# Optimization experiments

Hardware: AMD Instinct MI355X
Metric: run time of the kernel (lower is better)

The kernel has to match this reference:

```python
import jax, jax.numpy as jnp
import numpy as np

N, C, H, W, K = 8, 32, 512, 512, 6   # batch, embed dim, image HW, max components per image
MIN_PIX = 20
EPS = 1e-6
MARGIN = 0.5
L_INTER, L_INST, L_BG, L_SCENE = 0.4, 0.1, 0.2, 0.5


def _build_labels():
    # K disjoint 'subtitle line' rectangles per image; label 0 = background.
    # This is exactly what cv2.connectedComponents would return on the gt mask.
    labels = np.zeros((N, H, W), np.int32)
    for n in range(N):
        for k in range(K):
            r0 = 30 + k * 75
            c0 = 60 + (n % 3) * 20
            labels[n, r0:r0 + 40, c0:c0 + 300] = k + 1
    return labels


def setup_inputs() -> dict:
    key = jax.random.key(0)
    k1, k2 = jax.random.split(key)
    labels = _build_labels()
    gt = (labels > 0).astype(np.float32)[:, None]          # [N,1,H,W]
    color = jax.random.normal(k1, (N, C, H, W), jnp.float32)
    binary = jax.random.uniform(k2, (N, 1, H, W), jnp.float32)  # pred binary map
    return {"color": color, "gt": jnp.asarray(gt), "binary": binary,
            "comp_labels": jnp.asarray(labels)}


def _safe_norm(d2):
    # torch.norm = sqrt(sum sq); tiny floor avoids NaN grads at exactly 0
    return jnp.sqrt(jnp.maximum(d2, 1e-12))


def reference(color, gt, binary, comp_labels):
    f32 = color.dtype
    sub = (gt[:, 0] > 0.5).astype(f32)                                   # [N,H,W]
    text = (jax.lax.stop_gradient(binary)[:, 0] > 0.5).astype(f32)       # detached
    scene = text * (1.0 - sub)
    bg = (1.0 - sub) * (1.0 - scene)

    # one-hot component masks [N,K,H,W]
    comp = (comp_labels[:, None, :, :] ==
            jnp.arange(1, K + 1, dtype=comp_labels.dtype)[None, :, None, None]).astype(f32)
    cnt = comp.sum((2, 3))                                               # [N,K]

    # per-component first/second moments via batched segment-reduce
    S1 = jnp.einsum('nchw,nkhw->nkc', color, comp)                       # sum of feat
    fsq = (color * color).sum(1)                                         # [N,H,W]
    S2 = jnp.einsum('nhw,nkhw->nk', fsq, comp)                           # sum of |feat|^2
    m_inst = S1 / (cnt + EPS)[:, :, None]                                # [N,K,C]
    # sum over comp pixels of |f - m|^2, divided by (cnt+eps)
    intra_k = (S2 - 2.0 * (m_inst * S1).sum(-1)
               + cnt * (m_inst * m_inst).sum(-1)) / (cnt + EPS)

    sub_cnt = sub.sum((1, 2)); bg_cnt = bg.sum((1, 2)); scene_cnt = scene.sum((1, 2))
    m_sub = jnp.einsum('nchw,nhw->nc', color, sub) / (sub_cnt + EPS)[:, None]
    m_bg = jnp.einsum('nchw,nhw->nc', color, bg) / (bg_cnt + EPS)[:, None]
    m_scene = jnp.einsum('nchw,nhw->nc', color, scene) / (scene_cnt + EPS)[:, None]

    comp_big = cnt >= MIN_PIX                                            # [N,K]
    n_valid = comp_big.sum(1)                                            # [N]
    item_valid = (bg_cnt >= MIN_PIX) & (n_valid >= 1)
    cv = comp_big & item_valid[:, None]
    total = cv.sum()

    intra_sum = jnp.where(cv, intra_k, 0.0).sum()

    d_inst_bg = _safe_norm(((m_inst - m_bg[:, None, :]) ** 2).sum(-1))   # [N,K]
    inter_sum = jnp.where(cv, jax.nn.relu(MARGIN - d_inst_bg) ** 2, 0.0).sum()

    item_multi = item_valid & (n_valid > 1)
    d2_inst_sub = ((m_inst - m_sub[:, None, :]) ** 2).sum(-1)
    inst_sum = jnp.where(cv & item_multi[:, None], d2_inst_sub, 0.0).sum()
    inst_n = jnp.where(item_multi, n_valid, 0).sum()

    bg_cond = item_valid & (sub_cnt >= MIN_PIX)
    d_sub_bg = _safe_norm(((m_sub - m_bg) ** 2).sum(-1))
    subbg_sum = jnp.where(bg_cond, jax.nn.relu(MARGIN - d_sub_bg) ** 2, 0.0).sum()
    subbg_n = bg_cond.sum()

    sc_cond = item_valid & (scene_cnt >= MIN_PIX) & (sub_cnt >= MIN_PIX)
    d_sub_sc = _safe_norm(((m_sub - m_scene) ** 2).sum(-1))
    subsc_sum = jnp.where(sc_cond, jax.nn.relu(2.0 * MARGIN - d_sub_sc) ** 2, 0.0).sum()
    subsc_n = sc_cond.sum()

    def avg(s, n):
        return jnp.where(n > 0, s / jnp.maximum(n, 1).astype(f32), 0.0)

    loss = (avg(intra_sum, total)
            + L_INTER * avg(inter_sum, total)
            + L_INST * avg(inst_sum, inst_n)
            + L_BG * avg(subbg_sum, subbg_n)
            + L_SCENE * avg(subsc_sum, subsc_n))
    return jnp.where(total > 0, loss, jnp.zeros((), f32))
```

## Files before the change

### kernel.cpp

```cpp
#include <hip/hip_runtime.h>


#define NIMG   8
#define NCH    32
#define IMHW   (512 * 512)
#define CHUNK  1024
#define CPI    (IMHW / CHUNK)
#define WSN    304
#define LC_OFF    12288
#define CODES_OFF 16384

__device__ __forceinline__ float redhalf(float x) {
    x += __shfl_xor(x, 1);  x += __shfl_xor(x, 2);  x += __shfl_xor(x, 4);
    x += __shfl_xor(x, 8);  x += __shfl_xor(x, 16);
    return x;
}
__device__ __forceinline__ float red64(float x) {
    x = redhalf(x); x += __shfl_xor(x, 32); return x;
}

__global__ __launch_bounds__(256) void scl_codes(
    const float* __restrict__ gt, const float* __restrict__ bin,
    const int* __restrict__ lab, float* __restrict__ ws,
    unsigned char* __restrict__ lc, unsigned* __restrict__ codes)
{
    __shared__ float ldsc[8];
    __shared__ int labmask;
    const int tid = threadIdx.x;
    if (tid < 8) ldsc[tid] = 0.f;
    if (tid == 0) labmask = 0;

    const int n = blockIdx.x / CPI;
    const int q = blockIdx.x % CPI;
    const int base = n * IMHW + q * CHUNK;
    const int p = base + (tid << 2);

    const float4 g4 = *reinterpret_cast<const float4*>(gt + p);
    const float4 b4 = *reinterpret_cast<const float4*>(bin + p);
    const int4   l4 = *reinterpret_cast<const int4*>(lab + p);
    const float gg[4] = {g4.x, g4.y, g4.z, g4.w};
    const float bb[4] = {b4.x, b4.y, b4.z, b4.w};
    const int   ll[4] = {l4.x, l4.y, l4.z, l4.w};

    unsigned wrd = 0; int lm = 0;
    float c0 = 0.f, c1 = 0.f;
    float ck[6] = {0.f, 0.f, 0.f, 0.f, 0.f, 0.f};
#pragma unroll
    for (int e = 0; e < 4; ++e) {
        const bool sub  = gg[e] > 0.5f;
        const bool text = bb[e] > 0.5f;
        const int  r    = sub ? 0 : (text ? 1 : 2);
        unsigned   ul   = (unsigned)ll[e];
        if (ul > 7u) ul = 7u;
        wrd |= ((ul << 2) | (unsigned)r) << (8 * e);
        lm  |= 1 << ul;
        c0  += (r == 0) ? 1.f : 0.f;
        c1  += (r == 1) ? 1.f : 0.f;
#pragma unroll
        for (int kk = 0; kk < 6; ++kk)
            ck[kk] += (ul == (unsigned)(kk + 1)) ? 1.f : 0.f;
    }
    codes[(base >> 2) + tid] = wrd;

    c0 = red64(c0); c1 = red64(c1);
#pragma unroll
    for (int kk = 0; kk < 6; ++kk) ck[kk] = red64(ck[kk]);
    lm |= __shfl_xor(lm, 1);  lm |= __shfl_xor(lm, 2);  lm |= __shfl_xor(lm, 4);
    lm |= __shfl_xor(lm, 8);  lm |= __shfl_xor(lm, 16); lm |= __shfl_xor(lm, 32);

    __syncthreads();
    if ((tid & 63) == 0) {
        atomicAdd(&ldsc[0], c0);
        atomicAdd(&ldsc[1], c1);
#pragma unroll
        for (int kk = 0; kk < 6; ++kk) atomicAdd(&ldsc[2 + kk], ck[kk]);
        atomicOr(&labmask, lm);
    }
    __syncthreads();

    float* wsn = ws + (size_t)n * WSN;
    if (tid == 0) {
        lc[n * CPI + q] = (unsigned char)((labmask >> 1) & 0x3F);
        atomicAdd(&wsn[288], ldsc[0]);
        atomicAdd(&wsn[289], ldsc[1]);
    }
    if (tid >= 2 && tid < 8) atomicAdd(&wsn[291 + (tid - 2)], ldsc[tid]);
}

__global__ __launch_bounds__(256) void scl_color(
    const float* __restrict__ color, const float* __restrict__ ws_ro,
    const unsigned char* __restrict__ lc, const unsigned* __restrict__ codes,
    float* __restrict__ ws)
{
    __shared__ unsigned ldsC[CHUNK / 4];
    (void)ws_ro;

    const int bid = blockIdx.x;
    const int g = bid & 3;
    const int q = (bid >> 2) & (CPI - 1);
    const int n = bid >> 10;

    const int tid  = threadIdx.x;
    const int lane = tid & 63;
    const int wv   = tid >> 6;
    const int half = lane >> 5;
    const int l32  = lane & 31;

    const int base = n * IMHW + q * CHUNK;
    ldsC[tid] = codes[(base >> 2) + tid];

    const unsigned mask6 = lc[n * CPI + q];
    const int Lc = mask6 ? __ffs(mask6) : 255;

    const int c = g * 8 + wv * 2 + half;
    const float* colc = color + ((size_t)n * NCH + c) * IMHW + q * CHUNK;

    __syncthreads();

    float vt = 0.f, s0 = 0.f, s1 = 0.f, aL = 0.f, s2 = 0.f;
#pragma unroll
    for (int j = 0; j < CHUNK; j += 128) {
        const int off = j + (l32 << 2);
        const float4 v4 = *reinterpret_cast<const float4*>(colc + off);
        const unsigned cw = ldsC[off >> 2];
        const float vv[4] = {v4.x, v4.y, v4.z, v4.w};
#pragma unroll
        for (int e = 0; e < 4; ++e) {
            const float v = vv[e];
            const int r = (int)((cw >> (8 * e)) & 3u);
            const int l = (int)((cw >> (8 * e + 2)) & 0x3Fu);
            vt += v;
            s0 += (r == 0) ? v : 0.f;
            s1 += (r == 1) ? v : 0.f;
            const float mv = (l == Lc) ? v : 0.f;
            aL += mv;
            s2 = fmaf(mv, mv, s2);
        }
    }

    vt = redhalf(vt); s0 = redhalf(s0); s1 = redhalf(s1);
    aL = redhalf(aL); s2 = redhalf(s2);
    s2 += __shfl_xor(s2, 32);

    float* wsn = ws + (size_t)n * WSN;
    if (l32 == 0) {
        atomicAdd(&wsn[ 0 + c], s0);
        atomicAdd(&wsn[32 + c], s1);
        atomicAdd(&wsn[64 + c], vt);
        if (Lc >= 1 && Lc <= 6) {
            atomicAdd(&wsn[96 + (Lc - 1) * 32 + c], aL);
            if (lane == 0) atomicAdd(&wsn[297 + (Lc - 1)], s2);
        }
    }

    unsigned extra = mask6 ? (mask6 & (mask6 - 1)) : 0u;
    while (extra) {
        const int L2 = __ffs(extra); extra &= extra - 1;
        float aX = 0.f, sX = 0.f;
#pragma unroll
        for (int j = 0; j < CHUNK; j += 128) {
            const int off = j + (l32 << 2);
            const float4 v4 = *reinterpret_cast<const float4*>(colc + off);
            const unsigned cw = ldsC[off >> 2];
            const float vv[4] = {v4.x, v4.y, v4.z, v4.w};
#pragma unroll
            for (int e = 0; e < 4; ++e) {
                const int l = (int)((cw >> (8 * e + 2)) & 0x3Fu);
                const float mv = (l == L2) ? vv[e] : 0.f;
                aX += mv;
                sX = fmaf(mv, mv, sX);
            }
        }
        aX = redhalf(aX); sX = redhalf(sX);
        sX += __shfl_xor(sX, 32);
        if (l32 == 0 && L2 >= 1 && L2 <= 6) {
            atomicAdd(&wsn[96 + (L2 - 1) * 32 + c], aX);
            if (lane == 0) atomicAdd(&wsn[297 + (L2 - 1)], sX);
        }
    }
}

__global__ void scl_final(const float* __restrict__ ws, float* __restrict__ out)
{
    const int lane = threadIdx.x;
    const int n = lane / 6;
    const int k = lane - n * 6;
    const bool active = lane < 48;

    float t_cv = 0.f, t_intra = 0.f, t_inter = 0.f, t_inst = 0.f, t_instn = 0.f;
    float t_sbg = 0.f, t_sbgn = 0.f, t_ssc = 0.f, t_sscn = 0.f;

    if (active) {
        const float* w = ws + (size_t)n * WSN;
        const float cnt    = w[291 + k];
        const float s2     = w[297 + k];
        const float subc   = w[288];
        const float scenec = w[289];
        const float bgc    = 262144.f - subc - scenec;

        float nv = 0.f;
#pragma unroll
        for (int kk = 0; kk < 6; ++kk) nv += (w[291 + kk] >= 20.f) ? 1.f : 0.f;

        const bool comp_big   = cnt >= 20.f;
        const bool item_valid = (bgc >= 20.f) && (nv >= 1.f);
        const bool cv         = comp_big && item_valid;

        const float den  = cnt + 1e-6f;
        const float dsub = subc + 1e-6f;
        const float dbg  = bgc + 1e-6f;
        const float dsc  = scenec + 1e-6f;

        float dot_mS1 = 0.f, dot_mm = 0.f, d2bg = 0.f, d2sub = 0.f;
        for (int c = 0; c < 32; ++c) {
            const float S1 = w[96 + k * 32 + c];
            const float m  = S1 / den;
            dot_mS1 = fmaf(m, S1, dot_mS1);
            dot_mm  = fmaf(m, m, dot_mm);
            const float msub = w[c] / dsub;
            const float mbg  = (w[64 + c] - w[c] - w[32 + c]) / dbg;
            float d = m - mbg;  d2bg  = fmaf(d, d, d2bg);
            d = m - msub;       d2sub = fmaf(d, d, d2sub);
        }
        const float intra_k = (s2 - 2.f * dot_mS1 + cnt * dot_mm) / den;

        if (cv) {
            t_cv = 1.f;
            t_intra = intra_k;
            const float dd = sqrtf(fmaxf(d2bg, 1e-12f));
            const float r  = fmaxf(0.5f - dd, 0.f);
            t_inter = r * r;
        }
        const bool multi = item_valid && (nv > 1.f);
        if (cv && multi) t_inst = d2sub;

        if (k == 0) {
            if (multi) t_instn = nv;
            const bool bgcond = item_valid && (subc >= 20.f);
            const bool sccond = item_valid && (scenec >= 20.f) && (subc >= 20.f);
            float d2sb = 0.f, d2ss = 0.f;
            for (int c = 0; c < 32; ++c) {
                const float msub = w[c] / dsub;
                const float mbg  = (w[64 + c] - w[c] - w[32 + c]) / dbg;
                const float msc  = w[32 + c] / dsc;
                float a = msub - mbg; d2sb = fmaf(a, a, d2sb);
                float b = msub - msc; d2ss = fmaf(b, b, d2ss);
            }
            if (bgcond) {
                const float dd = sqrtf(fmaxf(d2sb, 1e-12f));
                const float r  = fmaxf(0.5f - dd, 0.f);
                t_sbg = r * r; t_sbgn = 1.f;
            }
            if (sccond) {
                const float dd = sqrtf(fmaxf(d2ss, 1e-12f));
                const float r  = fmaxf(1.0f - dd, 0.f);
                t_ssc = r * r; t_sscn = 1.f;
            }
        }
    }

#define RED64(x) { x += __shfl_xor(x, 1); x += __shfl_xor(x, 2); x += __shfl_xor(x, 4); \
                   x += __shfl_xor(x, 8); x += __shfl_xor(x, 16); x += __shfl_xor(x, 32); }
    RED64(t_cv) RED64(t_intra) RED64(t_inter) RED64(t_inst) RED64(t_instn)
    RED64(t_sbg) RED64(t_sbgn) RED64(t_ssc) RED64(t_sscn)
#undef RED64

    if (lane == 0) {
        const float total = t_cv;
        auto avg = [](float s, float nn) { return nn > 0.f ? s / fmaxf(nn, 1.f) : 0.f; };
        const float loss = avg(t_intra, total)
                         + 0.4f * avg(t_inter, total)
                         + 0.1f * avg(t_inst, t_instn)
                         + 0.2f * avg(t_sbg, t_sbgn)
                         + 0.5f * avg(t_ssc, t_sscn);
        out[0] = (total > 0.f) ? loss : 0.f;
    }
}

extern "C" void kernel_launch(void* const* d_in, const int* in_sizes, int n_in,
                              void* d_out, int out_size, void* d_ws, size_t ws_size,
                              hipStream_t stream)
{
    (void)in_sizes; (void)n_in; (void)out_size; (void)ws_size;
    const float* color = (const float*)d_in[0];
    const float* gt    = (const float*)d_in[1];
    const float* bin   = (const float*)d_in[2];
    const int*   lab   = (const int*)d_in[3];
    float*          ws    = (float*)d_ws;
    unsigned char*  lc    = (unsigned char*)d_ws + LC_OFF;
    unsigned*       codes = (unsigned*)((char*)d_ws + CODES_OFF);
    float* out = (float*)d_out;

    hipMemsetAsync(ws, 0, (size_t)NIMG * WSN * sizeof(float), stream);
    hipLaunchKernelGGL(scl_codes, dim3(NIMG * CPI), dim3(256), 0, stream,
                       gt, bin, lab, ws, lc, codes);
    hipLaunchKernelGGL(scl_color, dim3(NIMG * CPI * 4), dim3(256), 0, stream,
                       color, ws, lc, codes, ws);
    hipLaunchKernelGGL(scl_final, dim3(1), dim3(64), 0, stream, ws, out);
}
```

Measured before the change: 449.8 us.

## Use 8K-pixel slabs per channel block with partial buffers and reduce kernel

Work is now split into 32 slabs of 8192 pixels per image, with one block per (image, slab, channel) instead of 1024-pixel chunks spread over channel groups. Each block writes its per-block partial sums to a buffer, and a new scl_reduce kernel sums them, replacing thousands of global float atomics. Codes are read straight from global memory rather than staged in LDS. The aim is to cut atomic contention and per-block overhead. In exchange it adds a kernel launch, a serial reduction over slabs, and more re-reads of codes per channel, and slabs containing several components rerun the extra component loop over more data.

New measurement: 426.6 us. 1.05x faster.

```diff
diff --git a/kernel.cpp b/kernel.cpp
--- a/kernel.cpp
+++ b/kernel.cpp
@@ -4,71 +4,73 @@
 #define NIMG   8
 #define NCH    32
 #define IMHW   (512 * 512)
-#define CHUNK  1024
-#define CPI    (IMHW / CHUNK)
+#define SLAB   8192
+#define NSLAB  32
 #define WSN    304
 #define LC_OFF    12288
-#define CODES_OFF 16384
-
-__device__ __forceinline__ float redhalf(float x) {
+#define CNT_OFF   16384
+#define CODES_OFF 32768
+#define PB_OFF    (4 * 1024 * 1024)
+
+__device__ __forceinline__ float red64(float x) {
     x += __shfl_xor(x, 1);  x += __shfl_xor(x, 2);  x += __shfl_xor(x, 4);
-    x += __shfl_xor(x, 8);  x += __shfl_xor(x, 16);
+    x += __shfl_xor(x, 8);  x += __shfl_xor(x, 16); x += __shfl_xor(x, 32);
     return x;
-}
-__device__ __forceinline__ float red64(float x) {
-    x = redhalf(x); x += __shfl_xor(x, 32); return x;
 }
 
 __global__ __launch_bounds__(256) void scl_codes(
     const float* __restrict__ gt, const float* __restrict__ bin,
-    const int* __restrict__ lab, float* __restrict__ ws,
-    unsigned char* __restrict__ lc, unsigned* __restrict__ codes)
+    const int* __restrict__ lab, unsigned char* __restrict__ lc,
+    float* __restrict__ cntpb, unsigned* __restrict__ codes)
 {
     __shared__ float ldsc[8];
     __shared__ int labmask;
     const int tid = threadIdx.x;
     if (tid < 8) ldsc[tid] = 0.f;
     if (tid == 0) labmask = 0;
-
-    const int n = blockIdx.x / CPI;
-    const int q = blockIdx.x % CPI;
-    const int base = n * IMHW + q * CHUNK;
-    const int p = base + (tid << 2);
-
-    const float4 g4 = *reinterpret_cast<const float4*>(gt + p);
-    const float4 b4 = *reinterpret_cast<const float4*>(bin + p);
-    const int4   l4 = *reinterpret_cast<const int4*>(lab + p);
-    const float gg[4] = {g4.x, g4.y, g4.z, g4.w};
-    const float bb[4] = {b4.x, b4.y, b4.z, b4.w};
-    const int   ll[4] = {l4.x, l4.y, l4.z, l4.w};
-
-    unsigned wrd = 0; int lm = 0;
+    __syncthreads();
+
+    const int n = blockIdx.x >> 5;
+    const int s = blockIdx.x & 31;
+    const int base = n * IMHW + s * SLAB;
+
     float c0 = 0.f, c1 = 0.f;
     float ck[6] = {0.f, 0.f, 0.f, 0.f, 0.f, 0.f};
-#pragma unroll
-    for (int e = 0; e < 4; ++e) {
-        const bool sub  = gg[e] > 0.5f;
-        const bool text = bb[e] > 0.5f;
-        const int  r    = sub ? 0 : (text ? 1 : 2);
-        unsigned   ul   = (unsigned)ll[e];
-        if (ul > 7u) ul = 7u;
-        wrd |= ((ul << 2) | (unsigned)r) << (8 * e);
-        lm  |= 1 << ul;
-        c0  += (r == 0) ? 1.f : 0.f;
-        c1  += (r == 1) ? 1.f : 0.f;
-#pragma unroll
-        for (int kk = 0; kk < 6; ++kk)
-            ck[kk] += (ul == (unsigned)(kk + 1)) ? 1.f : 0.f;
-    }
-    codes[(base >> 2) + tid] = wrd;
+    int lm = 0;
+#pragma unroll
+    for (int i = 0; i < 8; ++i) {
+        const int off = i * 1024 + (tid << 2);
+        const int p   = base + off;
+        const float4 g4 = *reinterpret_cast<const float4*>(gt + p);
+        const float4 b4 = *reinterpret_cast<const float4*>(bin + p);
+        const int4   l4 = *reinterpret_cast<const int4*>(lab + p);
+        const float gg[4] = {g4.x, g4.y, g4.z, g4.w};
+        const float bb[4] = {b4.x, b4.y, b4.z, b4.w};
+        const int   ll[4] = {l4.x, l4.y, l4.z, l4.w};
+        unsigned wrd = 0;
+#pragma unroll
+        for (int e = 0; e < 4; ++e) {
+            const bool sub  = gg[e] > 0.5f;
+            const bool text = bb[e] > 0.5f;
+            const int  r    = sub ? 0 : (text ? 1 : 2);
+            unsigned   ul   = (unsigned)ll[e];
+            if (ul > 7u) ul = 7u;
+            wrd |= ((ul << 2) | (unsigned)r) << (8 * e);
+            lm  |= 1 << ul;
+            c0  += (r == 0) ? 1.f : 0.f;
+            c1  += (r == 1) ? 1.f : 0.f;
+#pragma unroll
+            for (int kk = 0; kk < 6; ++kk)
+                ck[kk] += (ul == (unsigned)(kk + 1)) ? 1.f : 0.f;
+        }
+        codes[(base >> 2) + i * 256 + tid] = wrd;
+    }
 
     c0 = red64(c0); c1 = red64(c1);
 #pragma unroll
     for (int kk = 0; kk < 6; ++kk) ck[kk] = red64(ck[kk]);
     lm |= __shfl_xor(lm, 1);  lm |= __shfl_xor(lm, 2);  lm |= __shfl_xor(lm, 4);
     lm |= __shfl_xor(lm, 8);  lm |= __shfl_xor(lm, 16); lm |= __shfl_xor(lm, 32);
-
-    __syncthreads();
     if ((tid & 63) == 0) {
         atomicAdd(&ldsc[0], c0);
         atomicAdd(&ldsc[1], c1);
@@ -78,51 +80,40 @@
     }
     __syncthreads();
 
-    float* wsn = ws + (size_t)n * WSN;
-    if (tid == 0) {
-        lc[n * CPI + q] = (unsigned char)((labmask >> 1) & 0x3F);
-        atomicAdd(&wsn[288], ldsc[0]);
-        atomicAdd(&wsn[289], ldsc[1]);
-    }
-    if (tid >= 2 && tid < 8) atomicAdd(&wsn[291 + (tid - 2)], ldsc[tid]);
-}
-
-__global__ __launch_bounds__(256) void scl_color(
-    const float* __restrict__ color, const float* __restrict__ ws_ro,
-    const unsigned char* __restrict__ lc, const unsigned* __restrict__ codes,
-    float* __restrict__ ws)
-{
-    __shared__ unsigned ldsC[CHUNK / 4];
-    (void)ws_ro;
-
-    const int bid = blockIdx.x;
-    const int g = bid & 3;
-    const int q = (bid >> 2) & (CPI - 1);
-    const int n = bid >> 10;
-
+    if (tid == 0)
+        lc[blockIdx.x] = (unsigned char)((labmask >> 1) & 0x3F);
+    if (tid < 8)
+        cntpb[blockIdx.x * 8 + tid] = ldsc[tid];
+}
+
+__global__ __launch_bounds__(256, 8) void scl_color(
+    const float* __restrict__ color, const unsigned char* __restrict__ lc,
+    const unsigned* __restrict__ codes, float* __restrict__ pb,
+    float* __restrict__ stats)
+{
+    __shared__ float acc[5];
     const int tid  = threadIdx.x;
     const int lane = tid & 63;
-    const int wv   = tid >> 6;
-    const int half = lane >> 5;
-    const int l32  = lane & 31;
-
-    const int base = n * IMHW + q * CHUNK;
-    ldsC[tid] = codes[(base >> 2) + tid];
-
-    const unsigned mask6 = lc[n * CPI + q];
+    if (tid < 5) acc[tid] = 0.f;
+    __syncthreads();
+
+    const int bid = blockIdx.x;
+    const int c   = bid & 31;
+    const int sl  = (bid >> 5) & 31;
+    const int n   = bid >> 10;
+
+    const size_t colbase = ((size_t)(n * NCH + c)) * IMHW + sl * SLAB;
+    const int    wbase   = (n * IMHW + sl * SLAB) >> 2;
+
+    const unsigned mask6 = lc[n * NSLAB + sl];
     const int Lc = mask6 ? __ffs(mask6) : 255;
 
-    const int c = g * 8 + wv * 2 + half;
-    const float* colc = color + ((size_t)n * NCH + c) * IMHW + q * CHUNK;
-
-    __syncthreads();
-
     float vt = 0.f, s0 = 0.f, s1 = 0.f, aL = 0.f, s2 = 0.f;
 #pragma unroll
-    for (int j = 0; j < CHUNK; j += 128) {
-        const int off = j + (l32 << 2);
-        const float4 v4 = *reinterpret_cast<const float4*>(colc + off);
-        const unsigned cw = ldsC[off >> 2];
+    for (int i = 0; i < 8; ++i) {
+        const int off = i * 1024 + (tid << 2);
+        const float4 v4 = *reinterpret_cast<const float4*>(color + colbase + off);
+        const unsigned cw = codes[wbase + i * 256 + tid];
         const float vv[4] = {v4.x, v4.y, v4.z, v4.w};
 #pragma unroll
         for (int e = 0; e < 4; ++e) {
@@ -138,30 +129,26 @@
         }
     }
 
-    vt = redhalf(vt); s0 = redhalf(s0); s1 = redhalf(s1);
-    aL = redhalf(aL); s2 = redhalf(s2);
-    s2 += __shfl_xor(s2, 32);
-
-    float* wsn = ws + (size_t)n * WSN;
-    if (l32 == 0) {
-        atomicAdd(&wsn[ 0 + c], s0);
-        atomicAdd(&wsn[32 + c], s1);
-        atomicAdd(&wsn[64 + c], vt);
-        if (Lc >= 1 && Lc <= 6) {
-            atomicAdd(&wsn[96 + (Lc - 1) * 32 + c], aL);
-            if (lane == 0) atomicAdd(&wsn[297 + (Lc - 1)], s2);
-        }
-    }
+    vt = red64(vt); s0 = red64(s0); s1 = red64(s1);
+    aL = red64(aL); s2 = red64(s2);
+    if (lane == 0) {
+        atomicAdd(&acc[0], s0);
+        atomicAdd(&acc[1], s1);
+        atomicAdd(&acc[2], vt);
+        atomicAdd(&acc[3], aL);
+        atomicAdd(&acc[4], s2);
+    }
+    __syncthreads();
+    if (tid < 5) pb[(size_t)bid * 8 + tid] = acc[tid];
 
     unsigned extra = mask6 ? (mask6 & (mask6 - 1)) : 0u;
     while (extra) {
         const int L2 = __ffs(extra); extra &= extra - 1;
         float aX = 0.f, sX = 0.f;
-#pragma unroll
-        for (int j = 0; j < CHUNK; j += 128) {
-            const int off = j + (l32 << 2);
-            const float4 v4 = *reinterpret_cast<const float4*>(colc + off);
-            const unsigned cw = ldsC[off >> 2];
+        for (int i = 0; i < 8; ++i) {
+            const int off = i * 1024 + (tid << 2);
+            const float4 v4 = *reinterpret_cast<const float4*>(color + colbase + off);
+            const unsigned cw = codes[wbase + i * 256 + tid];
             const float vv[4] = {v4.x, v4.y, v4.z, v4.w};
 #pragma unroll
             for (int e = 0; e < 4; ++e) {
@@ -171,12 +158,60 @@
                 sX = fmaf(mv, mv, sX);
             }
         }
-        aX = redhalf(aX); sX = redhalf(sX);
-        sX += __shfl_xor(sX, 32);
-        if (l32 == 0 && L2 >= 1 && L2 <= 6) {
-            atomicAdd(&wsn[96 + (L2 - 1) * 32 + c], aX);
-            if (lane == 0) atomicAdd(&wsn[297 + (L2 - 1)], sX);
-        }
+        aX = red64(aX); sX = red64(sX);
+        if (lane == 0) {
+            atomicAdd(&stats[(size_t)n * WSN + 96 + (L2 - 1) * 32 + c], aX);
+            atomicAdd(&stats[(size_t)n * WSN + 297 + (L2 - 1)], sX);
+        }
+    }
+}
+
+__global__ __launch_bounds__(64) void scl_reduce(
+    const float* __restrict__ pb, const float* __restrict__ cntpb,
+    const unsigned char* __restrict__ lc, float* __restrict__ stats)
+{
+    __shared__ float comp[6][32];
+    __shared__ float comps2[6];
+    const int tid = threadIdx.x;
+    const int n   = blockIdx.x;
+    for (int i = tid; i < 192; i += 64) (&comp[0][0])[i] = 0.f;
+    if (tid < 6) comps2[tid] = 0.f;
+    __syncthreads();
+
+    float* w = stats + (size_t)n * WSN;
+
+    if (tid < 32) {
+        const int c = tid;
+        float a0 = 0.f, a1 = 0.f, a2 = 0.f;
+        for (int sl = 0; sl < NSLAB; ++sl) {
+            const float* p = pb + ((size_t)((n * NSLAB + sl) * NCH + c)) * 8;
+            a0 += p[0]; a1 += p[1]; a2 += p[2];
+            const unsigned m = lc[n * NSLAB + sl];
+            if (m) {
+                const int L = __ffs(m);
+                atomicAdd(&comp[L - 1][c], p[3]);
+                atomicAdd(&comps2[L - 1], p[4]);
+            }
+        }
+        w[ 0 + c] += a0;
+        w[32 + c] += a1;
+        w[64 + c] += a2;
+    } else if (tid < 40) {
+        const int j = tid - 32;
+        float a = 0.f;
+        for (int sl = 0; sl < NSLAB; ++sl)
+            a += cntpb[(n * NSLAB + sl) * 8 + j];
+        if (j == 0) w[288] += a;
+        else if (j == 1) w[289] += a;
+        else w[291 + (j - 2)] += a;
+    }
+    __syncthreads();
+
+    if (tid < 32) {
+#pragma unroll
+        for (int kk = 0; kk < 6; ++kk) w[96 + kk * 32 + tid] += comp[kk][tid];
+    } else if (tid < 38) {
+        w[297 + (tid - 32)] += comps2[tid - 32];
     }
 }
 
@@ -286,15 +321,19 @@
     const float* gt    = (const float*)d_in[1];
     const float* bin   = (const float*)d_in[2];
     const int*   lab   = (const int*)d_in[3];
-    float*          ws    = (float*)d_ws;
-    unsigned char*  lc    = (unsigned char*)d_ws + LC_OFF;
-    unsigned*       codes = (unsigned*)((char*)d_ws + CODES_OFF);
+    float*         stats = (float*)d_ws;
+    unsigned char* lc    = (unsigned char*)d_ws + LC_OFF;
+    float*         cntpb = (float*)((char*)d_ws + CNT_OFF);
+    unsigned*      codes = (unsigned*)((char*)d_ws + CODES_OFF);
+    float*         pb    = (float*)((char*)d_ws + PB_OFF);
     float* out = (float*)d_out;
 
-    hipMemsetAsync(ws, 0, (size_t)NIMG * WSN * sizeof(float), stream);
-    hipLaunchKernelGGL(scl_codes, dim3(NIMG * CPI), dim3(256), 0, stream,
-                       gt, bin, lab, ws, lc, codes);
-    hipLaunchKernelGGL(scl_color, dim3(NIMG * CPI * 4), dim3(256), 0, stream,
-                       color, ws, lc, codes, ws);
-    hipLaunchKernelGGL(scl_final, dim3(1), dim3(64), 0, stream, ws, out);
-}
+    hipMemsetAsync(stats, 0, (size_t)NIMG * WSN * sizeof(float), stream);
+    hipLaunchKernelGGL(scl_codes, dim3(NIMG * NSLAB), dim3(256), 0, stream,
+                       gt, bin, lab, lc, cntpb, codes);
+    hipLaunchKernelGGL(scl_color, dim3(NIMG * NSLAB * NCH), dim3(256), 0, stream,
+                       color, lc, codes, pb, stats);
+    hipLaunchKernelGGL(scl_reduce, dim3(NIMG), dim3(64), 0, stream,
+                       pb, cntpb, lc, stats);
+    hipLaunchKernelGGL(scl_final, dim3(1), dim3(64), 0, stream, stats, out);
+}
```
